# Optimization experiments

Measured on AMD Instinct MI355X. Metric: run time of the kernel, lower is better.

Reference implementation:

```python
import jax, jax.numpy as jnp
import numpy as np

DIM = 10  # GMM components == feature dim


def _conv(x, w, b):
    y = jax.lax.conv_general_dilated(x, w, window_strides=(1, 1), padding='VALID',
                                     dimension_numbers=('NCHW', 'OIHW', 'NCHW'))
    return y + b[None, :, None, None]


def _gmm(x, centers, raw_mats):
    # x: [B, d]; centers: [K, d]; raw_mats: [K, d, d] with K == d == DIM
    K, d = centers.shape
    I = jnp.eye(d, dtype=x.dtype)
    L = jnp.tril(raw_mats, -1) + I                       # unit lower-triangular [K,d,d]
    root_D = jnp.diagonal(raw_mats, axis1=-2, axis2=-1)  # [K,d]
    D = root_D * root_D + 1e-4
    # Sigma_inv = L^{-T} D^{-1} L^{-1}
    L_inv = jax.scipy.linalg.solve_triangular(L, jnp.broadcast_to(I, L.shape), lower=True)
    Sigma_inv = jnp.einsum('kai,ka,kaj->kij', L_inv, 1.0 / D, L_inv)
    det_scale = jax.lax.rsqrt(jnp.prod(D, axis=-1))      # [K]
    diff = x[:, None, :] - centers[None, :, :]           # [B,K,d]
    dist_sq = jnp.einsum('bkd,kde,bke->bk', diff, Sigma_inv, diff)
    expo = -0.5 * dist_sq
    expo_safe = expo - jnp.max(expo, axis=1, keepdims=True)
    numer = det_scale[None, :] * jnp.exp(expo_safe)
    return numer / jnp.sum(numer, axis=1, keepdims=True)


def setup_inputs() -> dict:
    key = jax.random.key(0)
    ks = jax.random.split(key, 12)
    B = 4096
    x = jax.random.normal(ks[0], (B, 1, 28, 28), dtype=jnp.float32)
    conv1_w = jax.random.normal(ks[1], (32, 1, 3, 3), jnp.float32) * (1.0 / np.sqrt(1 * 9))
    conv1_b = jnp.zeros((32,), jnp.float32)
    conv2_w = jax.random.normal(ks[2], (64, 32, 3, 3), jnp.float32) * (1.0 / np.sqrt(32 * 9))
    conv2_b = jnp.zeros((64,), jnp.float32)
    fc1_w = jax.random.normal(ks[3], (128, 9216), jnp.float32) * (1.0 / np.sqrt(9216))
    fc1_b = jnp.zeros((128,), jnp.float32)
    fc2_w = jax.random.normal(ks[4], (DIM, 128), jnp.float32) * (1.0 / np.sqrt(128))
    fc2_b = jnp.zeros((DIM,), jnp.float32)
    centers = jax.random.normal(ks[5], (DIM, DIM), jnp.float32)
    raw_mats = jax.random.normal(ks[6], (DIM, DIM, DIM), jnp.float32) * 0.1 + jnp.eye(DIM)[None]
    return {'x': x, 'conv1_w': conv1_w, 'conv1_b': conv1_b, 'conv2_w': conv2_w,
            'conv2_b': conv2_b, 'fc1_w': fc1_w, 'fc1_b': fc1_b, 'fc2_w': fc2_w,
            'fc2_b': fc2_b, 'centers': centers, 'raw_mats': raw_mats}


def reference(x, conv1_w, conv1_b, conv2_w, conv2_b, fc1_w, fc1_b, fc2_w, fc2_b, centers, raw_mats):
    h = jax.nn.relu(_conv(x, conv1_w, conv1_b))          # [B,32,26,26]
    h = jax.nn.relu(_conv(h, conv2_w, conv2_b))          # [B,64,24,24]
    h = jax.lax.reduce_window(h, -jnp.inf, jax.lax.max, (1, 1, 2, 2), (1, 1, 2, 2), 'VALID')
    h = h.reshape(h.shape[0], -1)                        # [B,9216] (dropout = identity in eval)
    h = jax.nn.relu(h @ fc1_w.T + fc1_b)
    h = h @ fc2_w.T + fc2_b                              # [B,10]
    return _gmm(h, centers, raw_mats)
```

## Files before the change

kernel.cpp:

```cpp
#include <hip/hip_runtime.h>

typedef _Float16 half_t;
typedef _Float16 half8  __attribute__((ext_vector_type(8)));
typedef _Float16 half2v __attribute__((ext_vector_type(2)));
typedef float    floatx4 __attribute__((ext_vector_type(4)));

#define MFMA16(a, b, c) __builtin_amdgcn_mfma_f32_16x16x32_f16((a), (b), (c), 0, 0, 0)

__global__ void k_prep(const float* __restrict__ fw1, half_t* __restrict__ W1h,
                       const float* __restrict__ w2, half_t* __restrict__ W2T,
                       const float* __restrict__ raw, float* __restrict__ Sinv,
                       float* __restrict__ dets) {
    __shared__ float s_raw[1000];
    __shared__ float s_Li[1000];
    __shared__ float s_Dinv[100];
    const int blk = blockIdx.x;
    const int t = threadIdx.x;
    if (blk < 4608) {
        const int i = blk * 256 + t;
        W1h[i] = (half_t)fw1[i];
    } else if (blk < 4680) {
        const int i = (blk - 4608) * 256 + t;
        if (i < 18432) {
            const int tap = i / 2048;
            const int r = i - tap * 2048;
            const int co = r >> 5;
            const int ci = r & 31;
            W2T[i] = (half_t)w2[(co * 32 + ci) * 9 + tap];
        }
    } else {
        for (int i = t; i < 1000; i += 256) s_raw[i] = raw[i];
        __syncthreads();
        if (t < 100) {
            const int k = t / 10;
            const int j = t - k * 10;
            float v[10];
#pragma unroll
            for (int i = 0; i < 10; ++i) {
                float s = (i == j) ? 1.0f : 0.0f;
#pragma unroll
                for (int mm = 0; mm < 10; ++mm)
                    if (mm < i) s -= s_raw[k * 100 + i * 10 + mm] * v[mm];
                v[i] = s;
            }
#pragma unroll
            for (int a = 0; a < 10; ++a) s_Li[k * 100 + a * 10 + j] = v[a];
        } else if (t < 110) {
            const int k = t - 100;
            float prod = 1.0f;
#pragma unroll
            for (int a = 0; a < 10; ++a) {
                const float rd = s_raw[k * 100 + a * 10 + a];
                const float dv = rd * rd + 1e-4f;
                s_Dinv[k * 10 + a] = 1.0f / dv;
                prod *= dv;
            }
            dets[k] = rsqrtf(prod);
        }
        __syncthreads();
        for (int idx = t; idx < 1000; idx += 256) {
            const int k = idx / 100;
            const int r = idx - k * 100;
            const int ii = r / 10;
            const int jj = r - ii * 10;
            float s = 0.0f;
#pragma unroll
            for (int a = 0; a < 10; ++a)
                s += s_Li[k * 100 + a * 10 + ii] * s_Dinv[k * 10 + a] *
                     s_Li[k * 100 + a * 10 + jj];
            Sinv[idx] = s;
        }
    }
}

__global__ __launch_bounds__(256, 3) void k_convs(
    const float* __restrict__ x, const float* __restrict__ w1,
    const float* __restrict__ b1, const float* __restrict__ b2,
    const half_t* __restrict__ W2T, half_t* __restrict__ h2p) {
    __shared__ float s_x[784];
    __shared__ float s_w1[288];
    __shared__ float s_b1[32];
    __shared__ float s_b2[64];
    __shared__ __align__(16) half_t s_h1[688 * 32];

    const int t = threadIdx.x;
    const int b = blockIdx.x;

    for (int i = t; i < 784; i += 256) s_x[i] = x[(size_t)b * 784 + i];
    for (int i = t; i < 288; i += 256) s_w1[i] = w1[i];
    if (t < 32) s_b1[t] = b1[t];
    if (t < 64) s_b2[t] = b2[t];
    if (t < 384) s_h1[21632 + t] = (half_t)0.0f;
    __syncthreads();

    const int w = t >> 6;
    const int ln = t & 63;
    const int n16 = ln & 15;
    const int q = ln >> 4;

    {
        float wr[8][9], br[8];
#pragma unroll
        for (int j = 0; j < 8; ++j) {
            br[j] = s_b1[w * 8 + j];
#pragma unroll
            for (int k = 0; k < 9; ++k) wr[j][k] = s_w1[(w * 8 + j) * 9 + k];
        }
        for (int p = ln; p < 676; p += 64) {
            const int yy = p / 26;
            const int xx = p - yy * 26;
            float win[9];
#pragma unroll
            for (int r = 0; r < 3; ++r)
#pragma unroll
                for (int c = 0; c < 3; ++c) win[r * 3 + c] = s_x[(yy + r) * 28 + xx + c];
            half8 hv;
#pragma unroll
            for (int j = 0; j < 8; ++j) {
                float a = br[j];
#pragma unroll
                for (int k = 0; k < 9; ++k) a = fmaf(win[k], wr[j][k], a);
                hv[j] = (half_t)fmaxf(a, 0.0f);
            }
            *(half8*)((char*)s_h1 + ((p << 6) + (w << 4))) = hv;
        }
    }

    const int cp = w & 1;
    const int st = w >> 1;
    half8 bf[9][2];
#pragma unroll
    for (int tap = 0; tap < 9; ++tap)
#pragma unroll
        for (int cc = 0; cc < 2; ++cc)
            bf[tap][cc] = *(const half8*)(W2T +
                ((tap * 64 + (2 * cp + cc) * 16 + n16) * 32 + q * 8));

    __syncthreads();

#pragma unroll
    for (int tap = 0; tap < 9; ++tap)
#pragma unroll
        for (int cc = 0; cc < 2; ++cc)
            asm volatile("" : "+v"(bf[tap][cc]));

    const char* rp = (const char*)s_h1 + (((n16 + 16 * st) << 6) + (q << 4));

    const float bb0 = s_b2[cp * 32 + n16];
    const float bb1 = s_b2[cp * 32 + 16 + n16];
    half_t* outp = h2p + (size_t)b * 9216 + (size_t)(cp * 32 + n16) * 144 +
                   8 * st + 2 * q;
    const bool dostore = (st == 0) | (q < 2);

    const floatx4 z4 = {0.f, 0.f, 0.f, 0.f};
    floatx4 sl0[2] = {z4, z4}, sl1[2] = {z4, z4}, sl2[2] = {z4, z4};
    float yb00 = 0.f, yb01 = 0.f, yb10 = 0.f, yb11 = 0.f;

#define RETIRE(YO, AC)                                                        \
    do {                                                                      \
        const float p0 = fmaxf(AC[0][0], AC[0][1]);                           \
        const float p1 = fmaxf(AC[0][2], AC[0][3]);                           \
        const float r0 = fmaxf(AC[1][0], AC[1][1]);                           \
        const float r1 = fmaxf(AC[1][2], AC[1][3]);                           \
        if (((YO) & 1) == 0) {                                                \
            yb00 = p0; yb01 = p1; yb10 = r0; yb11 = r1;                       \
        } else if (dostore) {                                                 \
            half2v h0, h1v;                                                   \
            h0[0] = (half_t)fmaxf(fmaxf(yb00, p0) + bb0, 0.0f);               \
            h0[1] = (half_t)fmaxf(fmaxf(yb01, p1) + bb0, 0.0f);               \
            h1v[0] = (half_t)fmaxf(fmaxf(yb10, r0) + bb1, 0.0f);              \
            h1v[1] = (half_t)fmaxf(fmaxf(yb11, r1) + bb1, 0.0f);              \
            half_t* op = outp + ((YO) >> 1) * 12;                             \
            *(half2v*)(op) = h0;                                              \
            *(half2v*)(op + 2304) = h1v;                                      \
        }                                                                     \
        AC[0] = z4; AC[1] = z4;                                               \
    } while (0)

#define CSTEP(Y_, A0, A1, A2)                                                 \
    do {                                                                      \
        const int y_ = (Y_);                                                  \
        if (y_ < 26) {                                                        \
            const half8 f0 = *(const half8*)(rp);                             \
            const half8 f1 = *(const half8*)(rp + 64);                        \
            const half8 f2 = *(const half8*)(rp + 128);                       \
            if (y_ <= 23) {                 \
                A0[0] = MFMA16(f0, bf[0][0], A0[0]);                          \
                A0[1] = MFMA16(f0, bf[0][1], A0[1]);                          \
                A0[0] = MFMA16(f1, bf[1][0], A0[0]);                          \
                A0[1] = MFMA16(f1, bf[1][1], A0[1]);                          \
                A0[0] = MFMA16(f2, bf[2][0], A0[0]);                          \
                A0[1] = MFMA16(f2, bf[2][1], A0[1]);                          \
            }                                                                 \
            if (y_ >= 1 && y_ <= 24) {    \
                A1[0] = MFMA16(f0, bf[3][0], A1[0]);                          \
                A1[1] = MFMA16(f0, bf[3][1], A1[1]);                          \
                A1[0] = MFMA16(f1, bf[4][0], A1[0]);                          \
                A1[1] = MFMA16(f1, bf[4][1], A1[1]);                          \
                A1[0] = MFMA16(f2, bf[5][0], A1[0]);                          \
                A1[1] = MFMA16(f2, bf[5][1], A1[1]);                          \
            }                                                                 \
            if (y_ >= 2) {   \
                A2[0] = MFMA16(f0, bf[6][0], A2[0]);                          \
                A2[1] = MFMA16(f0, bf[6][1], A2[1]);                          \
                A2[0] = MFMA16(f1, bf[7][0], A2[0]);                          \
                A2[1] = MFMA16(f1, bf[7][1], A2[1]);                          \
                A2[0] = MFMA16(f2, bf[8][0], A2[0]);                          \
                A2[1] = MFMA16(f2, bf[8][1], A2[1]);                          \
                RETIRE(y_ - 2, A2);                                           \
            }                                                                 \
            rp += 1664;                                                       \
        }                                                                     \
    } while (0)

    for (int yb = 0; yb < 27; yb += 3) {
        CSTEP(yb + 0, sl0, sl2, sl1);
        CSTEP(yb + 1, sl1, sl0, sl2);
        CSTEP(yb + 2, sl2, sl1, sl0);
    }
#undef CSTEP
#undef RETIRE
}

__global__ __launch_bounds__(256) void k_fc1(const half_t* __restrict__ A,
                                             const half_t* __restrict__ W,
                                             half_t* __restrict__ part) {
    const int t = threadIdx.x;
    const int mb = blockIdx.x;
    const int kb = blockIdx.y;
    const int w = t >> 6, ln = t & 63, n16 = ln & 15, q = ln >> 4;

    const half_t* a0 = A + (size_t)(mb * 128 + w * 32 + n16) * 9216 + kb * 576 + q * 8;
    const half_t* a1 = a0 + (size_t)16 * 9216;
    const half_t* wp = W + (size_t)n16 * 9216 + kb * 576 + q * 8;

    floatx4 acc[2][8];
#pragma unroll
    for (int s = 0; s < 2; ++s)
#pragma unroll
        for (int nt = 0; nt < 8; ++nt) acc[s][nt] = (floatx4){0.f, 0.f, 0.f, 0.f};

    for (int kt = 0; kt < 18; ++kt) {
        const int ko = kt * 32;
        half8 af0 = *(const half8*)(a0 + ko);
        half8 af1 = *(const half8*)(a1 + ko);
#pragma unroll
        for (int nt = 0; nt < 8; ++nt) {
            half8 bfr = *(const half8*)(wp + (size_t)nt * 16 * 9216 + ko);
            acc[0][nt] = MFMA16(af0, bfr, acc[0][nt]);
            acc[1][nt] = MFMA16(af1, bfr, acc[1][nt]);
        }
    }
    const int rowbase = mb * 128 + w * 32;
#pragma unroll
    for (int s = 0; s < 2; ++s)
#pragma unroll
        for (int nt = 0; nt < 8; ++nt)
#pragma unroll
            for (int r = 0; r < 4; ++r) {
                const int row = rowbase + s * 16 + q * 4 + r;
                const int col = nt * 16 + n16;
                part[(size_t)kb * 524288 + (size_t)row * 128 + col] = (half_t)acc[s][nt][r];
            }
}

__global__ void k_fc1red(const half_t* __restrict__ part, const float* __restrict__ b,
                         half_t* __restrict__ h3) {
    const int idx = blockIdx.x * 256 + threadIdx.x;
    const int col = idx & 127;
    float s = 0.0f;
#pragma unroll
    for (int j = 0; j < 16; ++j) s += (float)part[(size_t)j * 524288 + idx];
    s = fmaxf(s + b[col], 0.0f);
    h3[idx] = (half_t)s;
}

__global__ __launch_bounds__(256) void k_fc2gmm(
    const half_t* __restrict__ h3, const float* __restrict__ fw,
    const float* __restrict__ fb, const float* __restrict__ cent,
    const float* __restrict__ Sinv, const float* __restrict__ dets,
    float* __restrict__ out) {
    __shared__ float sw[1280];
    __shared__ float sb[10];
    __shared__ float sc[100];
    __shared__ float ss[1000];
    __shared__ float sd[10];
    const int t = threadIdx.x;
    for (int i = t; i < 1280; i += 256) sw[i] = fw[i];
    if (t < 10) sb[t] = fb[t];
    if (t < 100) sc[t] = cent[t];
    for (int i = t; i < 1000; i += 256) ss[i] = Sinv[i];
    if (t < 10) sd[t] = dets[t];
    __syncthreads();

    const int bidx = blockIdx.x * 256 + t;
    half2v hh[64];
    const half2v* hp = (const half2v*)(h3 + (size_t)bidx * 128);
#pragma unroll
    for (int i = 0; i < 64; ++i) hh[i] = hp[i];

    float y[10];
#pragma unroll
    for (int o = 0; o < 10; ++o) {
        float a = sb[o];
#pragma unroll
        for (int k = 0; k < 64; ++k) {
            a = fmaf((float)hh[k][0], sw[o * 128 + 2 * k], a);
            a = fmaf((float)hh[k][1], sw[o * 128 + 2 * k + 1], a);
        }
        y[o] = a;
    }

    float expo[10];
    float mx = -3.402823466e38f;
#pragma unroll
    for (int k = 0; k < 10; ++k) {
        float d[10];
#pragma unroll
        for (int j = 0; j < 10; ++j) d[j] = y[j] - sc[k * 10 + j];
        float s = 0.0f;
#pragma unroll
        for (int i = 0; i < 10; ++i) {
            float r = 0.0f;
#pragma unroll
            for (int j = 0; j < 10; ++j) r = fmaf(ss[k * 100 + i * 10 + j], d[j], r);
            s = fmaf(d[i], r, s);
        }
        expo[k] = -0.5f * s;
        mx = fmaxf(mx, expo[k]);
    }
    float num[10];
    float sum = 0.0f;
#pragma unroll
    for (int k = 0; k < 10; ++k) {
        num[k] = sd[k] * __expf(expo[k] - mx);
        sum += num[k];
    }
    const float inv = 1.0f / sum;
#pragma unroll
    for (int k = 0; k < 10; ++k) out[(size_t)bidx * 10 + k] = num[k] * inv;
}

extern "C" void kernel_launch(void* const* d_in, const int* in_sizes, int n_in,
                              void* d_out, int out_size, void* d_ws, size_t ws_size,
                              hipStream_t stream) {
    const float* x = (const float*)d_in[0];
    const float* w1 = (const float*)d_in[1];
    const float* b1 = (const float*)d_in[2];
    const float* w2 = (const float*)d_in[3];
    const float* b2 = (const float*)d_in[4];
    const float* fw1 = (const float*)d_in[5];
    const float* fb1 = (const float*)d_in[6];
    const float* fw2 = (const float*)d_in[7];
    const float* fb2 = (const float*)d_in[8];
    const float* cen = (const float*)d_in[9];
    const float* raw = (const float*)d_in[10];
    float* out = (float*)d_out;

    char* ws = (char*)d_ws;
    half_t* W2T = (half_t*)(ws);
    half_t* W1h = (half_t*)(ws + 36864);
    half_t* h2p = (half_t*)(ws + 2396160);
    half_t* part = (half_t*)(ws + 77893632);
    half_t* h3h = (half_t*)(ws + 94670848);
    float* gS = (float*)(ws + 95719424);
    float* gD = (float*)(ws + 95723424);

    k_prep<<<4681, 256, 0, stream>>>(fw1, W1h, w2, W2T, raw, gS, gD);
    k_convs<<<4096, 256, 0, stream>>>(x, w1, b1, b2, W2T, h2p);
    k_fc1<<<dim3(32, 16), 256, 0, stream>>>(h2p, W1h, part);
    k_fc1red<<<2048, 256, 0, stream>>>(part, fb1, h3h);
    k_fc2gmm<<<16, 256, 0, stream>>>(h3h, fw2, fb2, cen, gS, gD, out);
}
```

Before: 242.0 us.

## Split conv1 shared buffer into channel-group planes and pack conv1 FMAs

Conv1 output in shared memory moves from a pixel-major layout with 64-byte rows to four separate planes, one per 8-channel group. Conv2 MFMA fragment reads therefore stride 16 bytes across pixels, which is meant to cut LDS bank conflicts on the hot loop. Conv1 arithmetic is rewritten with float2 vectors so the compiler can emit packed FMAs, and the fc1 K loop gets an unroll-by-2 hint. The padding-zeroing code is changed to match the new plane layout, at the cost of more complex shared-memory indexing.

```diff
diff --git a/kernel.cpp b/kernel.cpp
--- a/kernel.cpp
+++ b/kernel.cpp
@@ -4,6 +4,7 @@
 typedef _Float16 half8  __attribute__((ext_vector_type(8)));
 typedef _Float16 half2v __attribute__((ext_vector_type(2)));
 typedef float    floatx4 __attribute__((ext_vector_type(4)));
+typedef float    float2v __attribute__((ext_vector_type(2)));
 
 #define MFMA16(a, b, c) __builtin_amdgcn_mfma_f32_16x16x32_f16((a), (b), (c), 0, 0, 0)
 
@@ -90,7 +91,12 @@
     for (int i = t; i < 288; i += 256) s_w1[i] = w1[i];
     if (t < 32) s_b1[t] = b1[t];
     if (t < 64) s_b2[t] = b2[t];
-    if (t < 384) s_h1[21632 + t] = (half_t)0.0f;
+    if (t < 48) {
+        const int qq = t / 12;
+        const int pp = 676 + (t - qq * 12);
+        half8 z = {0, 0, 0, 0, 0, 0, 0, 0};
+        *(half8*)((char*)s_h1 + (qq * 11008 + (pp << 4))) = z;
+    }
     __syncthreads();
 
     const int w = t >> 6;
@@ -99,30 +105,38 @@
     const int q = ln >> 4;
 
     {
-        float wr[8][9], br[8];
-#pragma unroll
-        for (int j = 0; j < 8; ++j) {
-            br[j] = s_b1[w * 8 + j];
-#pragma unroll
-            for (int k = 0; k < 9; ++k) wr[j][k] = s_w1[(w * 8 + j) * 9 + k];
+        float2v wr2[4][9], br2[4];
+#pragma unroll
+        for (int m = 0; m < 4; ++m) {
+            br2[m][0] = s_b1[w * 8 + 2 * m];
+            br2[m][1] = s_b1[w * 8 + 2 * m + 1];
+#pragma unroll
+            for (int k = 0; k < 9; ++k) {
+                wr2[m][k][0] = s_w1[(w * 8 + 2 * m) * 9 + k];
+                wr2[m][k][1] = s_w1[(w * 8 + 2 * m + 1) * 9 + k];
+            }
         }
         for (int p = ln; p < 676; p += 64) {
             const int yy = p / 26;
             const int xx = p - yy * 26;
-            float win[9];
+            float2v a2[4] = {br2[0], br2[1], br2[2], br2[3]};
 #pragma unroll
             for (int r = 0; r < 3; ++r)
 #pragma unroll
-                for (int c = 0; c < 3; ++c) win[r * 3 + c] = s_x[(yy + r) * 28 + xx + c];
+                for (int c = 0; c < 3; ++c) {
+                    const float xv = s_x[(yy + r) * 28 + xx + c];
+                    const float2v xv2 = {xv, xv};
+#pragma unroll
+                    for (int m = 0; m < 4; ++m)
+                        a2[m] = xv2 * wr2[m][r * 3 + c] + a2[m];
+                }
             half8 hv;
 #pragma unroll
-            for (int j = 0; j < 8; ++j) {
-                float a = br[j];
-#pragma unroll
-                for (int k = 0; k < 9; ++k) a = fmaf(win[k], wr[j][k], a);
-                hv[j] = (half_t)fmaxf(a, 0.0f);
-            }
-            *(half8*)((char*)s_h1 + ((p << 6) + (w << 4))) = hv;
+            for (int m = 0; m < 4; ++m) {
+                hv[2 * m] = (half_t)fmaxf(a2[m][0], 0.0f);
+                hv[2 * m + 1] = (half_t)fmaxf(a2[m][1], 0.0f);
+            }
+            *(half8*)((char*)s_h1 + (w * 11008 + (p << 4))) = hv;
         }
     }
 
@@ -144,7 +158,7 @@
         for (int cc = 0; cc < 2; ++cc)
             asm volatile("" : "+v"(bf[tap][cc]));
 
-    const char* rp = (const char*)s_h1 + (((n16 + 16 * st) << 6) + (q << 4));
+    const char* rp = (const char*)s_h1 + (q * 11008 + ((n16 + 16 * st) << 4));
 
     const float bb0 = s_b2[cp * 32 + n16];
     const float bb1 = s_b2[cp * 32 + 16 + n16];
@@ -182,8 +196,8 @@
         const int y_ = (Y_);                                                  \
         if (y_ < 26) {                                                        \
             const half8 f0 = *(const half8*)(rp);                             \
-            const half8 f1 = *(const half8*)(rp + 64);                        \
-            const half8 f2 = *(const half8*)(rp + 128);                       \
+            const half8 f1 = *(const half8*)(rp + 16);                        \
+            const half8 f2 = *(const half8*)(rp + 32);                        \
             if (y_ <= 23) {                 \
                 A0[0] = MFMA16(f0, bf[0][0], A0[0]);                          \
                 A0[1] = MFMA16(f0, bf[0][1], A0[1]);                          \
@@ -209,7 +223,7 @@
                 A2[1] = MFMA16(f2, bf[8][1], A2[1]);                          \
                 RETIRE(y_ - 2, A2);                                           \
             }                                                                 \
-            rp += 1664;                                                       \
+            rp += 416;                                                        \
         }                                                                     \
     } while (0)
 
@@ -240,6 +254,7 @@
 #pragma unroll
         for (int nt = 0; nt < 8; ++nt) acc[s][nt] = (floatx4){0.f, 0.f, 0.f, 0.f};
 
+#pragma unroll 2
     for (int kt = 0; kt < 18; ++kt) {
         const int ko = kt * 32;
         half8 af0 = *(const half8*)(a0 + ko);
```

Result: slower. 247.0 us (+2.1%).

## Fuse fc1 split-K reduction into fc2+GMM tail and halve fc1 row tile

Applied to the files above, without the earlier changes.

Merges the split-K partial-sum reduction, bias and ReLU into the fc2+GMM kernel, so the intermediate h3 buffer and one kernel launch are no longer needed. The new tail kernel uses 64 blocks of 64 threads, one sample per thread, each reading 16 partial vectors. fc1 now covers 64 rows per block instead of 128 and launches twice as many blocks, which lowers per-wave register pressure and improves occupancy. In exchange, the weight fragments are reused across fewer rows, and the tail reads partials per thread with strided, uncoalesced access across a small grid.

```diff
diff --git a/kernel.cpp b/kernel.cpp
--- a/kernel.cpp
+++ b/kernel.cpp
@@ -230,85 +230,84 @@
     const int kb = blockIdx.y;
     const int w = t >> 6, ln = t & 63, n16 = ln & 15, q = ln >> 4;
 
-    const half_t* a0 = A + (size_t)(mb * 128 + w * 32 + n16) * 9216 + kb * 576 + q * 8;
-    const half_t* a1 = a0 + (size_t)16 * 9216;
+    const half_t* a0 = A + (size_t)(mb * 64 + w * 16 + n16) * 9216 + kb * 576 + q * 8;
     const half_t* wp = W + (size_t)n16 * 9216 + kb * 576 + q * 8;
 
-    floatx4 acc[2][8];
-#pragma unroll
-    for (int s = 0; s < 2; ++s)
-#pragma unroll
-        for (int nt = 0; nt < 8; ++nt) acc[s][nt] = (floatx4){0.f, 0.f, 0.f, 0.f};
-
+    floatx4 acc[8];
+#pragma unroll
+    for (int nt = 0; nt < 8; ++nt) acc[nt] = (floatx4){0.f, 0.f, 0.f, 0.f};
+
+#pragma unroll 2
     for (int kt = 0; kt < 18; ++kt) {
         const int ko = kt * 32;
-        half8 af0 = *(const half8*)(a0 + ko);
-        half8 af1 = *(const half8*)(a1 + ko);
+        half8 af = *(const half8*)(a0 + ko);
 #pragma unroll
         for (int nt = 0; nt < 8; ++nt) {
             half8 bfr = *(const half8*)(wp + (size_t)nt * 16 * 9216 + ko);
-            acc[0][nt] = MFMA16(af0, bfr, acc[0][nt]);
-            acc[1][nt] = MFMA16(af1, bfr, acc[1][nt]);
-        }
-    }
-    const int rowbase = mb * 128 + w * 32;
-#pragma unroll
-    for (int s = 0; s < 2; ++s)
-#pragma unroll
-        for (int nt = 0; nt < 8; ++nt)
-#pragma unroll
-            for (int r = 0; r < 4; ++r) {
-                const int row = rowbase + s * 16 + q * 4 + r;
-                const int col = nt * 16 + n16;
-                part[(size_t)kb * 524288 + (size_t)row * 128 + col] = (half_t)acc[s][nt][r];
-            }
-}
-
-__global__ void k_fc1red(const half_t* __restrict__ part, const float* __restrict__ b,
-                         half_t* __restrict__ h3) {
-    const int idx = blockIdx.x * 256 + threadIdx.x;
-    const int col = idx & 127;
-    float s = 0.0f;
-#pragma unroll
-    for (int j = 0; j < 16; ++j) s += (float)part[(size_t)j * 524288 + idx];
-    s = fmaxf(s + b[col], 0.0f);
-    h3[idx] = (half_t)s;
-}
-
-__global__ __launch_bounds__(256) void k_fc2gmm(
-    const half_t* __restrict__ h3, const float* __restrict__ fw,
-    const float* __restrict__ fb, const float* __restrict__ cent,
-    const float* __restrict__ Sinv, const float* __restrict__ dets,
-    float* __restrict__ out) {
+            acc[nt] = MFMA16(af, bfr, acc[nt]);
+        }
+    }
+    const int rowbase = mb * 64 + w * 16;
+#pragma unroll
+    for (int nt = 0; nt < 8; ++nt)
+#pragma unroll
+        for (int r = 0; r < 4; ++r) {
+            const int row = rowbase + q * 4 + r;
+            const int col = nt * 16 + n16;
+            part[(size_t)kb * 524288 + (size_t)row * 128 + col] = (half_t)acc[nt][r];
+        }
+}
+
+__global__ __launch_bounds__(64) void k_tail(
+    const half_t* __restrict__ part, const float* __restrict__ fb1,
+    const float* __restrict__ fw, const float* __restrict__ fb,
+    const float* __restrict__ cent, const float* __restrict__ Sinv,
+    const float* __restrict__ dets, float* __restrict__ out) {
     __shared__ float sw[1280];
+    __shared__ float sfb1[128];
     __shared__ float sb[10];
     __shared__ float sc[100];
     __shared__ float ss[1000];
     __shared__ float sd[10];
     const int t = threadIdx.x;
-    for (int i = t; i < 1280; i += 256) sw[i] = fw[i];
+    for (int i = t; i < 1280; i += 64) sw[i] = fw[i];
+    for (int i = t; i < 128; i += 64) sfb1[i] = fb1[i];
     if (t < 10) sb[t] = fb[t];
-    if (t < 100) sc[t] = cent[t];
-    for (int i = t; i < 1000; i += 256) ss[i] = Sinv[i];
+    for (int i = t; i < 100; i += 64) sc[i] = cent[i];
+    for (int i = t; i < 1000; i += 64) ss[i] = Sinv[i];
     if (t < 10) sd[t] = dets[t];
     __syncthreads();
 
-    const int bidx = blockIdx.x * 256 + t;
-    half2v hh[64];
-    const half2v* hp = (const half2v*)(h3 + (size_t)bidx * 128);
-#pragma unroll
-    for (int i = 0; i < 64; ++i) hh[i] = hp[i];
+    const int smp = blockIdx.x * 64 + t;
+    const half_t* ps = part + (size_t)smp * 128;
 
     float y[10];
 #pragma unroll
-    for (int o = 0; o < 10; ++o) {
-        float a = sb[o];
-#pragma unroll
-        for (int k = 0; k < 64; ++k) {
-            a = fmaf((float)hh[k][0], sw[o * 128 + 2 * k], a);
-            a = fmaf((float)hh[k][1], sw[o * 128 + 2 * k + 1], a);
-        }
-        y[o] = a;
+    for (int o = 0; o < 10; ++o) y[o] = sb[o];
+
+#pragma unroll
+    for (int g = 0; g < 4; ++g) {
+        float acc[32];
+#pragma unroll
+        for (int c = 0; c < 32; ++c) acc[c] = 0.0f;
+#pragma unroll
+        for (int kb = 0; kb < 16; ++kb) {
+            const half8* pk = (const half8*)(ps + (size_t)kb * 524288 + g * 32);
+#pragma unroll
+            for (int vv = 0; vv < 4; ++vv) {
+                const half8 v = pk[vv];
+#pragma unroll
+                for (int j = 0; j < 8; ++j) acc[vv * 8 + j] += (float)v[j];
+            }
+        }
+#pragma unroll
+        for (int c = 0; c < 32; ++c) {
+            const half_t hv = (half_t)fmaxf(acc[c] + sfb1[g * 32 + c], 0.0f);
+            const float hf = (float)hv;
+#pragma unroll
+            for (int o = 0; o < 10; ++o)
+                y[o] = fmaf(hf, sw[o * 128 + g * 32 + c], y[o]);
+        }
     }
 
     float expo[10];
@@ -338,7 +337,7 @@
     }
     const float inv = 1.0f / sum;
 #pragma unroll
-    for (int k = 0; k < 10; ++k) out[(size_t)bidx * 10 + k] = num[k] * inv;
+    for (int k = 0; k < 10; ++k) out[(size_t)smp * 10 + k] = num[k] * inv;
 }
 
 extern "C" void kernel_launch(void* const* d_in, const int* in_sizes, int n_in,
@@ -362,13 +361,11 @@
     half_t* W1h = (half_t*)(ws + 36864);
     half_t* h2p = (half_t*)(ws + 2396160);
     half_t* part = (half_t*)(ws + 77893632);
-    half_t* h3h = (half_t*)(ws + 94670848);
     float* gS = (float*)(ws + 95719424);
     float* gD = (float*)(ws + 95723424);
 
     k_prep<<<4681, 256, 0, stream>>>(fw1, W1h, w2, W2T, raw, gS, gD);
     k_convs<<<4096, 256, 0, stream>>>(x, w1, b1, b2, W2T, h2p);
-    k_fc1<<<dim3(32, 16), 256, 0, stream>>>(h2p, W1h, part);
-    k_fc1red<<<2048, 256, 0, stream>>>(part, fb1, h3h);
-    k_fc2gmm<<<16, 256, 0, stream>>>(h3h, fw2, fb2, cen, gS, gD, out);
-}
+    k_fc1<<<dim3(64, 16), 256, 0, stream>>>(h2p, W1h, part);
+    k_tail<<<64, 64, 0, stream>>>(part, fb1, fw2, fb2, cen, gS, gD, out);
+}
```

After: 292.9 us. 1.21x slower.
